# Kernel tuning notes

Hardware: AMD Instinct MI355X
Metric: run time of the kernel (lower is better)

The kernel has to match this reference:

```python
import jax, jax.numpy as jnp
import numpy as np

EPS = 1e-10
BETA = 1.0  # beta passed to VectorQuantizer in Encoder_conv


def _conv(x, w, b, stride, pad):
    # x: NCHW, w: OIHW
    y = jax.lax.conv_general_dilated(x, w, window_strides=stride, padding=pad,
                                     dimension_numbers=('NCHW', 'OIHW', 'NCHW'))
    if b is not None:
        y = y + b[None, :, None, None]
    return y


def _forward(x, w_in, b_in, w_h1, b_h1, w_h2, b_h2, w_h3, b_h3,
             r0_w1, r0_w2, r1_w1, r1_w2, emb):
    relu = jax.nn.relu
    h = relu(_conv(x, w_in, b_in, (2, 2), [(1, 1), (1, 1)]))      # [B,128,256,256]
    h = relu(_conv(h, w_h1, b_h1, (4, 4), [(2, 2), (2, 2)]))      # [B,256,64,64]
    h = relu(_conv(h, w_h2, b_h2, (4, 4), [(2, 2), (2, 2)]))      # [B,256,16,16]
    h = relu(_conv(h, w_h3, b_h3, (2, 2), [(1, 1), (1, 1)]))      # [B,256,8,8]
    # ResidualBlock with 2 Residual layers: relu->conv[1,3]->relu->conv[1,1], no bias
    for wa, wb in ((r0_w1, r0_w2), (r1_w1, r1_w2)):
        t = _conv(relu(h), wa, None, (1, 1), [(0, 0), (1, 1)])
        t = _conv(relu(t), wb, None, (1, 1), [(0, 0), (0, 0)])
        h = h + t
    h = relu(h)
    # VectorQuantizer
    lat = jnp.transpose(h, (0, 2, 3, 1))                          # [B,H,W,D]
    D = emb.shape[1]
    flat = lat.reshape(-1, D)                                     # [N,D]
    dist = (jnp.sum(flat * flat, axis=1, keepdims=True)
            + jnp.sum(emb * emb, axis=1)
            - 2.0 * flat @ emb.T)                                 # [N,K]
    idx = jnp.argmin(dist, axis=1)                                # [N]
    quant = emb[idx].reshape(lat.shape)                           # [B,H,W,D]
    sg = jax.lax.stop_gradient
    e_loss = jnp.mean((sg(quant) - lat) ** 2)
    q_loss = jnp.mean((quant - sg(lat)) ** 2)
    loss = q_loss + BETA * e_loss
    quant_st = lat + sg(quant - lat)                              # straight-through
    probs = jnp.mean(jax.nn.one_hot(idx, emb.shape[0], dtype=lat.dtype), axis=0)
    perplexity = jnp.exp(-jnp.sum(probs * jnp.log(probs + EPS)))
    return jnp.transpose(quant_st, (0, 3, 1, 2)), loss, perplexity


def setup_inputs() -> dict:
    key = jax.random.key(0)
    ks = jax.random.split(key, 14)
    C_in, C, K = 3, 256, 512
    s = 0.05
    f32 = jnp.float32
    return {
        'x':     jax.random.normal(ks[0], (8, C_in, 512, 512), f32),
        'w_in':  jax.random.normal(ks[1], (C // 2, C_in, 4, 4), f32) * s,
        'b_in':  jnp.zeros((C // 2,), f32),
        'w_h1':  jax.random.normal(ks[2], (C, C // 2, 7, 7), f32) * s,
        'b_h1':  jnp.zeros((C,), f32),
        'w_h2':  jax.random.normal(ks[3], (C, C, 7, 7), f32) * s,
        'b_h2':  jnp.zeros((C,), f32),
        'w_h3':  jax.random.normal(ks[4], (C, C, 3, 3), f32) * s,
        'b_h3':  jnp.zeros((C,), f32),
        'r0_w1': jax.random.normal(ks[5], (4 * C, C, 1, 3), f32) * s,
        'r0_w2': jax.random.normal(ks[6], (C, 4 * C, 1, 1), f32) * s,
        'r1_w1': jax.random.normal(ks[7], (4 * C, C, 1, 3), f32) * s,
        'r1_w2': jax.random.normal(ks[8], (C, 4 * C, 1, 1), f32) * s,
        'emb':   jax.random.uniform(ks[9], (K, C), f32, -1.0 / K, 1.0 / K),
    }


def reference(x, w_in, b_in, w_h1, b_h1, w_h2, b_h2, w_h3, b_h3,
              r0_w1, r0_w2, r1_w1, r1_w2, emb):
    return _forward(x, w_in, b_in, w_h1, b_h1, w_h2, b_h2, w_h3, b_h3,
                    r0_w1, r0_w2, r1_w1, r1_w2, emb)
```

## Files before the change

kernel.cpp:

```cpp
#include <hip/hip_runtime.h>
#include <hip/hip_bf16.h>

typedef __hip_bfloat16 bf16;
typedef __attribute__((ext_vector_type(4))) float f32x4;
typedef __attribute__((ext_vector_type(8))) short short8;

__device__ __forceinline__ float b2f(bf16 v) { return __bfloat162float(v); }
__device__ __forceinline__ ushort f2bu(float v)
{
    bf16 b = __float2bfloat16(v);
    return *(ushort*)&b;
}
__device__ __forceinline__ uint relu2(uint v)
{
    uint r = v;
    if (r & 0x8000u)     r &= 0xFFFF0000u;
    if (r & 0x80000000u) r &= 0x0000FFFFu;
    return r;
}
__device__ __forceinline__ uint packbf2(float a, float b)
{
    uint lo = f2bu(a), hi = f2bu(b);
    return lo | (hi << 16);
}

typedef const __attribute__((address_space(1))) unsigned int* as1_u32;
typedef __attribute__((address_space(3))) unsigned int* as3_u32;
__device__ __forceinline__ void gld16(const void* g, uint* l)
{
    __builtin_amdgcn_global_load_lds((as1_u32)g, (as3_u32)l, 16, 0, 0);
}

__global__ __launch_bounds__(256) void initw_k(
        const float* __restrict__ w_in, const float* __restrict__ w_h1,
        const float* __restrict__ w_h2, const float* __restrict__ w_h3,
        const float* __restrict__ r0w1, const float* __restrict__ r0w2,
        const float* __restrict__ r1w1, const float* __restrict__ r1w2,
        const float* __restrict__ emb,
        bf16* __restrict__ wp1, bf16* __restrict__ wpack2, bf16* __restrict__ wpack3,
        bf16* __restrict__ wp4, bf16* __restrict__ wpA0, bf16* __restrict__ wpA1,
        bf16* __restrict__ wpB0, bf16* __restrict__ wpB1,
        float* __restrict__ en, float* __restrict__ mse, int* __restrict__ hist,
        float* __restrict__ zpad)
{
    __shared__ ushort ls[12544];
    int b = blockIdx.x, t = threadIdx.x;

    if (b < 256) {
        const float* src = w_h1 + (size_t)b * 6272;
        for (int i = t; i < 6272; i += 256) ls[i] = f2bu(src[i]);
        __syncthreads();
        for (int e = t; e < 800; e += 256) {
            int tap = e >> 4, cib8 = e & 15;
            short8 v;
            #pragma unroll
            for (int cil = 0; cil < 8; ++cil)
                v[cil] = (tap < 49) ? (short)ls[(cib8 * 8 + cil) * 49 + tap] : (short)0;
            *(short8*)(wpack2 + ((size_t)(tap * 16 + cib8) * 256 + b) * 8) = v;
        }
        return;
    }
    if (b < 512) {
        int co = b - 256;
        const float* src = w_h2 + (size_t)co * 12544;
        for (int i = t; i < 12544; i += 256) ls[i] = f2bu(src[i]);
        __syncthreads();
        for (int e = t; e < 1600; e += 256) {
            int tap = e >> 5, cib8 = e & 31;
            short8 v;
            #pragma unroll
            for (int cil = 0; cil < 8; ++cil)
                v[cil] = (tap < 49) ? (short)ls[(cib8 * 8 + cil) * 49 + tap] : (short)0;
            *(short8*)(wpack3 + ((size_t)(tap * 32 + cib8) * 256 + co) * 8) = v;
        }
        return;
    }
    if (b < 768) {
        int co = b - 512;
        const float* src = w_h3 + (size_t)co * 2304;
        for (int i = t; i < 2304; i += 256) ls[i] = f2bu(src[i]);
        __syncthreads();
        for (int e = t; e < 288; e += 256) {
            int tap = e >> 5, cib8 = e & 31;
            short8 v;
            #pragma unroll
            for (int cil = 0; cil < 8; ++cil)
                v[cil] = (short)ls[(cib8 * 8 + cil) * 9 + tap];
            *(short8*)(wp4 + ((size_t)(tap * 32 + cib8) * 256 + co) * 8) = v;
        }
        return;
    }
    if (b < 2816) {
        int r = b - 768;
        int which = r >> 10;
        int co = r & 1023;
        const float* srcb = which ? r1w1 : r0w1;
        bf16* dstb = which ? wpA1 : wpA0;
        const float* src = srcb + (size_t)co * 768;
        for (int i = t; i < 768; i += 256) ls[i] = f2bu(src[i]);
        __syncthreads();
        if (t < 96) {
            int tap = t >> 5, cib8 = t & 31;
            short8 v;
            #pragma unroll
            for (int cil = 0; cil < 8; ++cil)
                v[cil] = (short)ls[(cib8 * 8 + cil) * 3 + tap];
            *(short8*)(dstb + ((size_t)(tap * 32 + cib8) * 1024 + co) * 8) = v;
        }
        return;
    }
    if (b < 3072) {
        int r = b - 2816;
        int which = r >> 7;
        const float* srcb = which ? r1w2 : r0w2;
        bf16* dstb = which ? wpB1 : wpB0;
        int c = (r & 127) * 256 + t;
        int cib8 = c >> 8, co = c & 255;
        const float* s = srcb + (size_t)co * 1024 + cib8 * 8;
        short8 v;
        #pragma unroll
        for (int cil = 0; cil < 8; ++cil) v[cil] = (short)f2bu(s[cil]);
        *(short8*)(dstb + (size_t)c * 8) = v;
        return;
    }
    if (b < 3104) {
        int i = (b - 3072) * 256 + t;
        int j = i & 7; int co = (i >> 3) & 127; int kb = i >> 10;
        int k = kb * 8 + j;
        wp1[i] = __float2bfloat16(k < 48 ? w_in[co * 48 + k] : 0.f);
        return;
    }
    if (b < 3106) {
        int row = (b - 3104) * 256 + t;
        const float4* e = (const float4*)(emb + (size_t)row * 256);
        float s = 0.f;
        for (int d4 = 0; d4 < 64; ++d4) {
            float4 v = e[d4];
            s += v.x * v.x + v.y * v.y + v.z * v.z + v.w * v.w;
        }
        en[row] = s;
        return;
    }
    if (t == 0) mse[0] = 0.f;
    for (int i = t; i < 512; i += 256) hist[i] = 0;
    if (t < 64) zpad[t] = 0.f;
}

__global__ __launch_bounds__(256) void conv1m_k(const float* __restrict__ x,
        const bf16* __restrict__ wp1, const float* __restrict__ bias,
        bf16* __restrict__ h1c)
{
    int bid = blockIdx.x;
    int pxt = bid & 511, img = bid >> 9;
    int tr = pxt >> 4, tc = pxt & 15;
    int oh0 = tr * 8, ow0 = tc * 16;
    const float* xi = x + (size_t)img * 786432;
    bf16* oT = h1c + (size_t)img * 8388608;

    int t = threadIdx.x;
    int wave = t >> 6, lane = t & 63;
    int quad = lane >> 4, l15 = lane & 15;

    __shared__ ushort xs[4 * 640];
    __shared__ ushort ot[128 * 136];

    int ihb = oh0 * 2 - 1, iwb = ow0 * 2 - 1;
    for (int i = t; i < 1836; i += 256) {
        int ci = i / 612; int r1 = i - ci * 612;
        int ihl = r1 / 34, iwl = r1 - ihl * 34;
        int ih = ihb + ihl, iw = iwb + iwl;
        float v = 0.f;
        if ((unsigned)ih < 512u && (unsigned)iw < 512u)
            v = xi[ci * 262144 + ih * 512 + iw];
        xs[ci * 640 + ihl * 35 + iwl] = f2bu(v);
    }
    for (int i = t; i < 640; i += 256) xs[3 * 640 + i] = 0;
    __syncthreads();

    f32x4 zero = {0.f, 0.f, 0.f, 0.f};
    f32x4 acc[8][2];
    #pragma unroll
    for (int m = 0; m < 8; ++m) { acc[m][0] = zero; acc[m][1] = zero; }

    int ci_b = quad >> 1;
    int kh0 = (quad & 1) * 2;
    int iwl0 = 2 * l15;

    #pragma unroll
    for (int ks = 0; ks < 2; ++ks) {
        union { short8 v; uint u[4]; } b[2];
        #pragma unroll
        for (int nt = 0; nt < 2; ++nt) {
            int py = wave * 2 + nt;
            int base = (ks * 2 + ci_b) * 640 + (2 * py + kh0) * 35 + iwl0;
            b[nt].u[0] = *(const uint*)&xs[base];
            b[nt].u[1] = *(const uint*)&xs[base + 2];
            b[nt].u[2] = *(const uint*)&xs[base + 35];
            b[nt].u[3] = *(const uint*)&xs[base + 37];
        }
        const bf16* abase = wp1 + ((size_t)(ks * 4 + quad) * 128 + l15) * 8;
        #pragma unroll
        for (int m = 0; m < 8; ++m) {
            short8 a = *(const short8*)(abase + m * 16 * 8);
            acc[m][0] = __builtin_amdgcn_mfma_f32_16x16x32_bf16(a, b[0].v, acc[m][0], 0, 0, 0);
            acc[m][1] = __builtin_amdgcn_mfma_f32_16x16x32_bf16(a, b[1].v, acc[m][1], 0, 0, 0);
        }
    }

    #pragma unroll
    for (int m = 0; m < 8; ++m) {
        int cobase = m * 16 + quad * 4;
        float b0 = bias[cobase], b1 = bias[cobase + 1];
        float b2 = bias[cobase + 2], b3 = bias[cobase + 3];
        #pragma unroll
        for (int nt = 0; nt < 2; ++nt) {
            int pxl = (wave * 2 + nt) * 16 + l15;
            uint w0 = packbf2(fmaxf(b0 + acc[m][nt][0], 0.f),
                              fmaxf(b1 + acc[m][nt][1], 0.f));
            uint w1 = packbf2(fmaxf(b2 + acc[m][nt][2], 0.f),
                              fmaxf(b3 + acc[m][nt][3], 0.f));
            *(uint*)&ot[pxl * 136 + cobase]     = w0;
            *(uint*)&ot[pxl * 136 + cobase + 2] = w1;
        }
    }
    __syncthreads();
    {
        int pxl = t >> 1, half = t & 1;
        int oh = oh0 + (pxl >> 4), ow = ow0 + (pxl & 15);
        size_t px = (size_t)(oh * 256 + ow);
        #pragma unroll
        for (int cb = 0; cb < 4; ++cb) {
            int c16 = half * 4 + cb;
            const uint4* src = (const uint4*)&ot[pxl * 136 + c16 * 16];
            uint4* dst = (uint4*)(oT + ((size_t)c16 * 65536 + px) * 16);
            dst[0] = src[0];
            dst[1] = src[1];
        }
    }
}

template <int IH, int OH, int CI, int SPLIT, int MODE>
__global__ __launch_bounds__(256, 2) void conv_mfma9_k(
        const bf16* __restrict__ inC, const bf16* __restrict__ wpack,
        const float* __restrict__ bias, float* __restrict__ outA,
        bf16* __restrict__ outT, const float* __restrict__ zpad)
{
    constexpr int TPD = OH / 8;
    constexpr int NT = TPD * TPD;
    constexpr int CPB = (CI / 16) / SPLIT;
    constexpr int CIB8 = CI / 8;
    constexpr int NPX = IH * IH;
    constexpr int SLOTS = 2496;

    int bid = blockIdx.x;
    int pxt = bid % NT;
    int rest = bid / NT;
    int img = rest & 7;
    int split = rest >> 3;
    int oh0 = (pxt / TPD) * 8, ow0 = (pxt % TPD) * 8;

    int t = threadIdx.x;
    int wave = t >> 6, lane = t & 63;
    int quad = lane >> 4, l15 = lane & 15;

    const bf16* inb = inC + (size_t)img * ((size_t)NPX * CI);

    __shared__ __align__(16) uint bufA[SLOTS * 4];
    __shared__ __align__(16) uint bufB[SLOTS * 4];

    f32x4 zero = {0.f, 0.f, 0.f, 0.f};
    f32x4 acc[4][4];
    #pragma unroll
    for (int a = 0; a < 4; ++a)
        #pragma unroll
        for (int b = 0; b < 4; ++b) acc[a][b] = zero;

    int ihb = oh0 * 4 - 2, iwb = ow0 * 4 - 2;
    int qxl = l15 & 7, pyl = l15 >> 3;
    int tap_par = quad >> 1, ci_half = quad & 1;

    int  srel[10];
    bool sval[10];
    #pragma unroll
    for (int it = 0; it < 10; ++it) {
        int sb = (it < 9) ? it * 256 + wave * 64 : 2304 + wave * 64;
        int p  = sb + lane;
        int pb = p << 4;
        int lb = pb ^ (((pb >> 7) & 7) << 4);
        int j  = lb >> 4;
        int pos = j >> 1, half = j & 1;
        int r = pos / 35, c = pos - r * 35;
        int ih = ihb + r, iw = iwb + c;
        sval[it] = (j < 2450) && ((unsigned)ih < (unsigned)IH)
                   && ((unsigned)iw < (unsigned)IH);
        srel[it] = (ih * IH + iw) * 16 + half * 8;
    }

    auto stage = [&](int ch, uint* dst) {
        const bf16* cbp = inb + (size_t)ch * NPX * 16;
        #pragma unroll
        for (int it = 0; it < 10; ++it) {
            if (it == 9 && wave >= 3) continue;
            int sb = (it < 9) ? it * 256 + wave * 64 : 2304 + wave * 64;
            const void* src = sval[it] ? (const void*)(cbp + srel[it])
                                       : (const void*)zpad;
            gld16(src, dst + sb * 4);
        }
    };

    int rbase = pyl * 4480 + qxl * 128 + ci_half * 16;
    int d1  = tap_par * 32;
    int d29 = tap_par * 928;

    auto compute = [&](int ch, const uint* cbuf) {
        const bf16* ab = wpack
            + ((size_t)(ch * 2 + ci_half) * 256 + wave * 64 + l15) * 8
            + (size_t)tap_par * (CIB8 * 2048);
        __builtin_amdgcn_s_setprio(1);
        short8 aC[4], bC[4], aN[4], bN[4];
        {
            #pragma unroll
            for (int ct = 0; ct < 4; ++ct)
                aC[ct] = *(const short8*)(ab + ct * 128);
            int lbb = rbase + d1;
            #pragma unroll
            for (int pt = 0; pt < 4; ++pt) {
                int lb = lbb + pt * 8960;
                int pb = lb ^ (((lb >> 7) & 7) << 4);
                bC[pt] = *(const short8*)((const char*)cbuf + pb);
            }
        }
        #pragma unroll
        for (int tp = 0; tp < 25; ++tp) {
            if (tp < 24) {
                const int tn  = tp + 1;
                const int kh0 = (2 * tn) / 7, kw0 = (2 * tn) % 7;
                const int cE  = (kh0 * 35 + kw0) * 32;
                int dsel = (tn == 24) ? 0 : ((kw0 == 6) ? d29 : d1);
                int lbb  = rbase + cE + dsel;
                const bf16* at = ab + (size_t)(2 * tn) * (CIB8 * 2048);
                #pragma unroll
                for (int ct = 0; ct < 4; ++ct)
                    aN[ct] = *(const short8*)(at + ct * 128);
                #pragma unroll
                for (int pt = 0; pt < 4; ++pt) {
                    int lb = lbb + pt * 8960;
                    int pb = lb ^ (((lb >> 7) & 7) << 4);
                    bN[pt] = *(const short8*)((const char*)cbuf + pb);
                }
            }
            #pragma unroll
            for (int pt = 0; pt < 4; ++pt)
                #pragma unroll
                for (int ct = 0; ct < 4; ++ct)
                    acc[ct][pt] = __builtin_amdgcn_mfma_f32_16x16x32_bf16(
                        aC[ct], bC[pt], acc[ct][pt], 0, 0, 0);
            if (tp < 24) {
                #pragma unroll
                for (int i = 0; i < 4; ++i) { aC[i] = aN[i]; bC[i] = bN[i]; }
            }
        }
        __builtin_amdgcn_s_setprio(0);
    };

    if constexpr (CPB == 1) {
        stage(split, bufA);
        __syncthreads();
        compute(split, bufA);
    } else {
        stage(split * CPB, bufA);
        __syncthreads();
        for (int cc2 = 0; cc2 < CPB; cc2 += 2) {
            stage(split * CPB + cc2 + 1, bufB);
            compute(split * CPB + cc2, bufA);
            __syncthreads();
            if (cc2 + 2 < CPB) stage(split * CPB + cc2 + 2, bufA);
            compute(split * CPB + cc2 + 1, bufB);
            __syncthreads();
        }
    }

    #pragma unroll
    for (int ct = 0; ct < 4; ++ct) {
        int cobase = wave * 64 + ct * 16 + quad * 4;
        #pragma unroll
        for (int pt = 0; pt < 4; ++pt) {
            int px = pt * 16 + l15;
            int oh = oh0 + (px >> 3), ow = ow0 + (px & 7);
            int pxg = oh * OH + ow;
            #pragma unroll
            for (int r = 0; r < 4; ++r) {
                int co = cobase + r;
                float v = acc[ct][pt][r];
                if (MODE == 3) {
                    outA[(size_t)split * ((size_t)8 * OH * OH * 256)
                         + (size_t)img * (OH * OH * 256)
                         + (size_t)co * (OH * OH) + pxg] = v;
                } else {
                    float o = fmaxf(bias[co] + v, 0.f);
                    size_t base = (size_t)img * (size_t)(OH * OH * 256);
                    outT[base + ((size_t)(co >> 4) * (OH * OH) + pxg) * 16 + (co & 15)]
                        = __float2bfloat16(o);
                }
            }
        }
    }
}

__global__ void combine3_k(const float* __restrict__ p3, const float* __restrict__ bias,
                           bf16* __restrict__ h3T)
{
    int idx = blockIdx.x * 256 + threadIdx.x;
    int px = idx & 255;
    int co = (idx >> 8) & 255;
    int img = idx >> 16;
    float v = bias[co];
    #pragma unroll
    for (int s = 0; s < 16; ++s) v += p3[(size_t)s * 524288 + idx];
    v = fmaxf(v, 0.f);
    h3T[((size_t)img * 256 + px) * 256 + co] = __float2bfloat16(v);
}

__global__ __launch_bounds__(256) void conv4m_k(const bf16* __restrict__ h3T,
        const bf16* __restrict__ wp4, const float* __restrict__ bias,
        bf16* __restrict__ h4T)
{
    int bid = blockIdx.x;
    int img = bid >> 2, cog = bid & 3;
    int t = threadIdx.x;
    int wave = t >> 6, lane = t & 63;
    int quad = lane >> 4, l15 = lane & 15;

    __shared__ uint pt[16 * 325];

    for (int i = t; i < 16 * 325; i += 256) pt[i] = 0;

    f32x4 zero = {0.f, 0.f, 0.f, 0.f};
    f32x4 acc[4];
    #pragma unroll
    for (int b = 0; b < 4; ++b) acc[b] = zero;

    const bf16* inb = h3T + (size_t)img * 65536;

    for (int ch = 0; ch < 8; ++ch) {
        __syncthreads();
        for (int e = t; e < 4096; e += 256) {
            int cp = e & 15, px = e >> 4;
            int py = px >> 4, qx = px & 15;
            uint v = *(const uint*)(inb + (size_t)px * 256 + ch * 32 + cp * 2);
            pt[cp * 325 + (py + 1) * 18 + qx + 1] = v;
        }
        __syncthreads();

        for (int tap = 0; tap < 9; ++tap) {
            int kh = tap / 3, kw = tap - kh * 3;
            const bf16* abase = wp4 + ((size_t)((tap * 32 + ch * 4 + quad) * 256)
                                       + cog * 64 + wave * 16 + l15) * 8;
            short8 a = *(const short8*)abase;
            #pragma unroll
            for (int pq = 0; pq < 4; ++pq) {
                int pyo = 2 * pq + (l15 >> 3);
                int ipos = (2 * pyo + kh) * 18 + 2 * (l15 & 7) + kw;
                union { short8 v; uint u[4]; } b;
                b.u[0] = pt[(quad * 4 + 0) * 325 + ipos];
                b.u[1] = pt[(quad * 4 + 1) * 325 + ipos];
                b.u[2] = pt[(quad * 4 + 2) * 325 + ipos];
                b.u[3] = pt[(quad * 4 + 3) * 325 + ipos];
                acc[pq] = __builtin_amdgcn_mfma_f32_16x16x32_bf16(
                    a, b.v, acc[pq], 0, 0, 0);
            }
        }
    }

    int cobase = cog * 64 + wave * 16 + quad * 4;
    #pragma unroll
    for (int pq = 0; pq < 4; ++pq) {
        int px = pq * 16 + l15;
        #pragma unroll
        for (int r = 0; r < 4; ++r) {
            int co = cobase + r;
            float v = fmaxf(bias[co] + acc[pq][r], 0.f);
            h4T[((size_t)img * 64 + px) * 256 + co] = __float2bfloat16(v);
        }
    }
}

__global__ __launch_bounds__(256) void resam_k(const bf16* __restrict__ hT,
        const bf16* __restrict__ wpA, bf16* __restrict__ t1T)
{
    int bid = blockIdx.x;
    int img = bid >> 3, g = bid & 7;
    int t = threadIdx.x;
    int wave = t >> 6, lane = t & 63;
    int quad = lane >> 4, l15 = lane & 15;

    __shared__ uint ph[128 * 81];

    for (int i = t; i < 128 * 81; i += 256) ph[i] = 0;
    __syncthreads();
    const bf16* inb = hT + (size_t)img * 16384;
    for (int e = t; e < 8192; e += 256) {
        int cp = e & 127, px = e >> 7;
        uint v = relu2(*(const uint*)(inb + (size_t)px * 256 + cp * 2));
        ph[cp * 81 + (px >> 3) * 10 + (px & 7) + 1] = v;
    }
    __syncthreads();

    f32x4 zero = {0.f, 0.f, 0.f, 0.f};
    f32x4 acc[2][4];
    #pragma unroll
    for (int a = 0; a < 2; ++a)
        #pragma unroll
        for (int b = 0; b < 4; ++b) acc[a][b] = zero;

    for (int ch = 0; ch < 8; ++ch) {
        for (int tap = 0; tap < 3; ++tap) {
            const bf16* abase = wpA + ((size_t)(tap * 32 + ch * 4 + quad) * 1024
                                       + g * 128 + wave * 32 + l15) * 8;
            short8 a[2];
            #pragma unroll
            for (int ct = 0; ct < 2; ++ct)
                a[ct] = *(const short8*)(abase + ct * 16 * 8);
            #pragma unroll
            for (int pq = 0; pq < 4; ++pq) {
                int py = 2 * pq + (l15 >> 3);
                int pos = py * 10 + (l15 & 7) + tap;
                union { short8 v; uint u[4]; } b;
                b.u[0] = ph[(ch * 16 + quad * 4 + 0) * 81 + pos];
                b.u[1] = ph[(ch * 16 + quad * 4 + 1) * 81 + pos];
                b.u[2] = ph[(ch * 16 + quad * 4 + 2) * 81 + pos];
                b.u[3] = ph[(ch * 16 + quad * 4 + 3) * 81 + pos];
                #pragma unroll
                for (int ct = 0; ct < 2; ++ct)
                    acc[ct][pq] = __builtin_amdgcn_mfma_f32_16x16x32_bf16(
                        a[ct], b.v, acc[ct][pq], 0, 0, 0);
            }
        }
    }

    #pragma unroll
    for (int ct = 0; ct < 2; ++ct) {
        int cobase = g * 128 + wave * 32 + ct * 16 + quad * 4;
        #pragma unroll
        for (int pq = 0; pq < 4; ++pq) {
            int px = pq * 16 + l15;
            #pragma unroll
            for (int r = 0; r < 4; ++r)
                t1T[((size_t)img * 64 + px) * 1024 + cobase + r]
                    = __float2bfloat16(acc[ct][pq][r]);
        }
    }
}

__global__ __launch_bounds__(256) void resbm_k(const bf16* __restrict__ holdT,
        const bf16* __restrict__ t1T, const bf16* __restrict__ wpB,
        bf16* __restrict__ hnewT)
{
    int bid = blockIdx.x;
    int img = bid >> 2, cog = bid & 3;
    int t = threadIdx.x;
    int wave = t >> 6, lane = t & 63;
    int quad = lane >> 4, l15 = lane & 15;

    __shared__ uint pb[256 * 65];

    f32x4 zero = {0.f, 0.f, 0.f, 0.f};
    f32x4 acc[4];
    #pragma unroll
    for (int b = 0; b < 4; ++b) acc[b] = zero;

    const bf16* inb = t1T + (size_t)img * 65536;

    for (int s = 0; s < 2; ++s) {
        __syncthreads();
        for (int e = t; e < 16384; e += 256) {
            int cp = e & 255, px = e >> 8;
            uint v = relu2(*(const uint*)(inb + (size_t)px * 1024 + s * 512 + cp * 2));
            pb[cp * 65 + px] = v;
        }
        __syncthreads();

        for (int chl = 0; chl < 16; ++chl) {
            int ch = s * 16 + chl;
            const bf16* abase = wpB + ((size_t)(ch * 4 + quad) * 256
                                       + cog * 64 + wave * 16 + l15) * 8;
            short8 a = *(const short8*)abase;
            #pragma unroll
            for (int pq = 0; pq < 4; ++pq) {
                int px = pq * 16 + l15;
                union { short8 v; uint u[4]; } b;
                b.u[0] = pb[(chl * 16 + quad * 4 + 0) * 65 + px];
                b.u[1] = pb[(chl * 16 + quad * 4 + 1) * 65 + px];
                b.u[2] = pb[(chl * 16 + quad * 4 + 2) * 65 + px];
                b.u[3] = pb[(chl * 16 + quad * 4 + 3) * 65 + px];
                acc[pq] = __builtin_amdgcn_mfma_f32_16x16x32_bf16(
                    a, b.v, acc[pq], 0, 0, 0);
            }
        }
    }

    int cobase = cog * 64 + wave * 16 + quad * 4;
    #pragma unroll
    for (int pq = 0; pq < 4; ++pq) {
        int px = pq * 16 + l15;
        #pragma unroll
        for (int r = 0; r < 4; ++r) {
            int co = cobase + r;
            size_t o = ((size_t)img * 64 + px) * 256 + co;
            float v = b2f(holdT[o]) + acc[pq][r];
            hnewT[o] = __float2bfloat16(v);
        }
    }
}

__global__ __launch_bounds__(256) void vq_k(const bf16* __restrict__ h6T,
        const float* __restrict__ emb, const float* __restrict__ en,
        float* __restrict__ out, float* __restrict__ mse_acc, int* __restrict__ hist)
{
    int row0 = blockIdx.x * 4;
    int t = threadIdx.x;
    int wave = t >> 6, lane = t & 63;
    __shared__ float lat[4][256];
    __shared__ float swd[4][4];
    __shared__ int   swi[4][4];
    __shared__ int   fidx[4];
    __shared__ float smse[4];

    for (int e = t; e < 1024; e += 256) {
        int r = e >> 8, c = e & 255;
        lat[r][c] = fmaxf(b2f(h6T[(size_t)(row0 + r) * 256 + c]), 0.f);
    }
    __syncthreads();

    float a0[4] = {0.f, 0.f, 0.f, 0.f}, a1[4] = {0.f, 0.f, 0.f, 0.f};
    const float4* e0 = (const float4*)(emb + (size_t)t * 256);
    const float4* e1 = (const float4*)(emb + (size_t)(t + 256) * 256);
    for (int d4 = 0; d4 < 64; ++d4) {
        float4 v0 = e0[d4], v1 = e1[d4];
        #pragma unroll
        for (int r = 0; r < 4; ++r) {
            float l0 = lat[r][d4 * 4], l1 = lat[r][d4 * 4 + 1];
            float l2 = lat[r][d4 * 4 + 2], l3 = lat[r][d4 * 4 + 3];
            a0[r] += l0 * v0.x + l1 * v0.y + l2 * v0.z + l3 * v0.w;
            a1[r] += l0 * v1.x + l1 * v1.y + l2 * v1.z + l3 * v1.w;
        }
    }
    float en0 = en[t], en1 = en[t + 256];
    float bd[4]; int bi[4];
    #pragma unroll
    for (int r = 0; r < 4; ++r) {
        float d0 = en0 - 2.f * a0[r], d1v = en1 - 2.f * a1[r];
        bd[r] = d0; bi[r] = t;
        if (d1v < bd[r]) { bd[r] = d1v; bi[r] = t + 256; }
    }
    #pragma unroll
    for (int s = 1; s < 64; s <<= 1) {
        #pragma unroll
        for (int r = 0; r < 4; ++r) {
            float od = __shfl_xor(bd[r], s);
            int   oi = __shfl_xor(bi[r], s);
            if (od < bd[r] || (od == bd[r] && oi < bi[r])) { bd[r] = od; bi[r] = oi; }
        }
    }
    if (lane == 0) {
        #pragma unroll
        for (int r = 0; r < 4; ++r) { swd[wave][r] = bd[r]; swi[wave][r] = bi[r]; }
    }
    __syncthreads();
    if (t < 4) {
        float best = swd[0][t]; int bidx = swi[0][t];
        for (int w = 1; w < 4; ++w) {
            float od = swd[w][t]; int oi = swi[w][t];
            if (od < best || (od == best && oi < bidx)) { best = od; bidx = oi; }
        }
        fidx[t] = bidx;
    }
    __syncthreads();

    float msel = 0.f;
    #pragma unroll
    for (int r = 0; r < 4; ++r) {
        int row = row0 + r;
        int b = row >> 6, y = (row >> 3) & 7, xx = row & 7;
        float q = emb[(size_t)fidx[r] * 256 + t];
        out[((size_t)(b * 256 + t) * 8 + y) * 8 + xx] = q;
        float diff = q - lat[r][t];
        msel += diff * diff;
    }
    #pragma unroll
    for (int s = 1; s < 64; s <<= 1) msel += __shfl_xor(msel, s);
    if (lane == 0) smse[wave] = msel;
    __syncthreads();
    if (t == 0) atomicAdd(mse_acc, smse[0] + smse[1] + smse[2] + smse[3]);
    if (t < 4) atomicAdd(&hist[fidx[t]], 1);
}

__global__ void final_k(const float* __restrict__ mse_acc, const int* __restrict__ hist,
                        float* __restrict__ out)
{
    __shared__ float sh[512];
    int t = threadIdx.x;
    float p = (float)hist[t] / 512.f;
    sh[t] = p * logf(p + 1e-10f);
    __syncthreads();
    for (int s = 256; s > 0; s >>= 1) {
        if (t < s) sh[t] += sh[t + s];
        __syncthreads();
    }
    if (t == 0) {
        float loss = 2.f * mse_acc[0] / (512.f * 256.f);
        float perp = expf(-sh[0]);
        out[131072] = loss;
        out[131073] = perp;
    }
}

extern "C" void kernel_launch(void* const* d_in, const int* in_sizes, int n_in,
                              void* d_out, int out_size, void* d_ws, size_t ws_size,
                              hipStream_t stream)
{
    const float* x    = (const float*)d_in[0];
    const float* w_in = (const float*)d_in[1];
    const float* b_in = (const float*)d_in[2];
    const float* w_h1 = (const float*)d_in[3];
    const float* b_h1 = (const float*)d_in[4];
    const float* w_h2 = (const float*)d_in[5];
    const float* b_h2 = (const float*)d_in[6];
    const float* w_h3 = (const float*)d_in[7];
    const float* b_h3 = (const float*)d_in[8];
    const float* r0w1 = (const float*)d_in[9];
    const float* r0w2 = (const float*)d_in[10];
    const float* r1w1 = (const float*)d_in[11];
    const float* r1w2 = (const float*)d_in[12];
    const float* emb  = (const float*)d_in[13];
    float* out = (float*)d_out;

    char* ws = (char*)d_ws;
    size_t off = 0;
    auto alloc = [&](size_t bytes) -> void* {
        void* p = ws + off;
        off += (bytes + 255) & ~(size_t)255;
        return p;
    };

    float* en  = (float*)alloc(512 * 4);
    float* mse = (float*)alloc(256);
    int*  hist = (int*)alloc(512 * 4);
    float* zpad = (float*)alloc(256);
    float* p3  = (float*)alloc(8388608ull * 4);
    bf16* h3T  = (bf16*)alloc(524288ull * 2);
    bf16* h4T  = (bf16*)alloc(131072ull * 2);
    bf16* t1T  = (bf16*)alloc(524288ull * 2);
    bf16* h5T  = (bf16*)alloc(131072ull * 2);
    bf16* h6T  = (bf16*)alloc(131072ull * 2);
    bf16* wp1  = (bf16*)alloc(8192ull * 2);
    bf16* wpack2 = (bf16*)alloc(1638400ull * 2);
    bf16* wpack3 = (bf16*)alloc(3276800ull * 2);
    bf16* wp4  = (bf16*)alloc(589824ull * 2);
    bf16* wpA0 = (bf16*)alloc(786432ull * 2);
    bf16* wpA1 = (bf16*)alloc(786432ull * 2);
    bf16* wpB0 = (bf16*)alloc(262144ull * 2);
    bf16* wpB1 = (bf16*)alloc(262144ull * 2);
    bf16* h2c  = (bf16*)alloc(8388608ull * 2);
    size_t base_end = off;

    const size_t H1F_B = 8388608ull * 8 * 2;
    size_t needT1 = base_end + H1F_B + 4096;
    bf16* h1c;
    int tier;
    if (ws_size >= needT1) {
        h1c = (bf16*)alloc(H1F_B);
        tier = 1;
    } else {
        h1c = (bf16*)alloc(8388608ull * 2);
        tier = 2;
    }

    initw_k<<<3107, 256, 0, stream>>>(w_in, w_h1, w_h2, w_h3, r0w1, r0w2, r1w1, r1w2,
        emb, wp1, wpack2, wpack3, wp4, wpA0, wpA1, wpB0, wpB1, en, mse, hist, zpad);

    if (tier == 1) {
        conv1m_k<<<4096, 256, 0, stream>>>(x, wp1, b_in, h1c);
        conv_mfma9_k<256, 64, 128, 1, 0><<<512, 256, 0, stream>>>(
            h1c, wpack2, b_h1, nullptr, h2c, zpad);
    } else {
        for (int n = 0; n < 8; ++n) {
            conv1m_k<<<512, 256, 0, stream>>>(x + (size_t)n * 786432, wp1, b_in, h1c);
            conv_mfma9_k<256, 64, 128, 1, 0><<<64, 256, 0, stream>>>(
                h1c, wpack2, b_h1, nullptr, h2c + (size_t)n * 1048576, zpad);
        }
    }

    conv_mfma9_k<64, 16, 256, 16, 3><<<512, 256, 0, stream>>>(
        h2c, wpack3, nullptr, p3, nullptr, zpad);
    combine3_k<<<2048, 256, 0, stream>>>(p3, b_h2, h3T);

    conv4m_k<<<32, 256, 0, stream>>>(h3T, wp4, b_h3, h4T);
    resam_k<<<64, 256, 0, stream>>>(h4T, wpA0, t1T);
    resbm_k<<<32, 256, 0, stream>>>(h4T, t1T, wpB0, h5T);
    resam_k<<<64, 256, 0, stream>>>(h5T, wpA1, t1T);
    resbm_k<<<32, 256, 0, stream>>>(h5T, t1T, wpB1, h6T);

    vq_k<<<128, 256, 0, stream>>>(h6T, emb, en, out, mse, hist);
    final_k<<<1, 512, 0, stream>>>(mse, hist, out);
}
```

Baseline: 464.4 us.

## Fuse tail stages into one persistent kernel with grid barriers, halve conv3 split-K

Replaces the chain of small tail kernels (combine, conv4, two residual blocks, VQ, final reduction) with a single 64-block persistent kernel that uses a global atomic barrier between stages. The goal is to remove repeated launch overhead and inter-kernel gaps on small, latency-bound stages. It also reduces conv3's split-K from 16 to 8 and halves the partial-sum buffer, giving fewer but longer conv3 blocks. The combine step now transposes through LDS. The spin barrier relies on all 64 blocks being co-resident, and the VQ stage now runs on 64 blocks instead of 128.

```diff
diff --git a/kernel.cpp b/kernel.cpp
--- a/kernel.cpp
+++ b/kernel.cpp
@@ -29,6 +29,28 @@
 __device__ __forceinline__ void gld16(const void* g, uint* l)
 {
     __builtin_amdgcn_global_load_lds((as1_u32)g, (as3_u32)l, 16, 0, 0);
+}
+
+__device__ __forceinline__ void gbar(int* bar, int nblk)
+{
+    __syncthreads();
+    if (threadIdx.x == 0) {
+        __threadfence();
+        int g = __hip_atomic_load(&bar[1], __ATOMIC_RELAXED, __HIP_MEMORY_SCOPE_AGENT);
+        int a = __hip_atomic_fetch_add(&bar[0], 1, __ATOMIC_ACQ_REL, __HIP_MEMORY_SCOPE_AGENT);
+        if (a == nblk - 1) {
+            __hip_atomic_store(&bar[0], 0, __ATOMIC_RELAXED, __HIP_MEMORY_SCOPE_AGENT);
+            __hip_atomic_store(&bar[1], g + 1, __ATOMIC_RELEASE, __HIP_MEMORY_SCOPE_AGENT);
+        } else {
+            for (int it = 0; it < (1 << 22); ++it) {
+                if (__hip_atomic_load(&bar[1], __ATOMIC_ACQUIRE,
+                                      __HIP_MEMORY_SCOPE_AGENT) != g) break;
+                __builtin_amdgcn_s_sleep(8);
+            }
+        }
+        __threadfence();
+    }
+    __syncthreads();
 }
 
 __global__ __launch_bounds__(256) void initw_k(
@@ -41,7 +63,7 @@
         bf16* __restrict__ wp4, bf16* __restrict__ wpA0, bf16* __restrict__ wpA1,
         bf16* __restrict__ wpB0, bf16* __restrict__ wpB1,
         float* __restrict__ en, float* __restrict__ mse, int* __restrict__ hist,
-        float* __restrict__ zpad)
+        float* __restrict__ zpad, int* __restrict__ bar)
 {
     __shared__ ushort ls[12544];
     int b = blockIdx.x, t = threadIdx.x;
@@ -144,6 +166,7 @@
     if (t == 0) mse[0] = 0.f;
     for (int i = t; i < 512; i += 256) hist[i] = 0;
     if (t < 64) zpad[t] = 0.f;
+    if (t < 2) bar[t] = 0;
 }
 
 __global__ __launch_bounds__(256) void conv1m_k(const float* __restrict__ x,
@@ -407,311 +430,307 @@
     }
 }
 
-__global__ void combine3_k(const float* __restrict__ p3, const float* __restrict__ bias,
-                           bf16* __restrict__ h3T)
-{
-    int idx = blockIdx.x * 256 + threadIdx.x;
-    int px = idx & 255;
-    int co = (idx >> 8) & 255;
-    int img = idx >> 16;
-    float v = bias[co];
-    #pragma unroll
-    for (int s = 0; s < 16; ++s) v += p3[(size_t)s * 524288 + idx];
-    v = fmaxf(v, 0.f);
-    h3T[((size_t)img * 256 + px) * 256 + co] = __float2bfloat16(v);
-}
-
-__global__ __launch_bounds__(256) void conv4m_k(const bf16* __restrict__ h3T,
-        const bf16* __restrict__ wp4, const float* __restrict__ bias,
-        bf16* __restrict__ h4T)
-{
-    int bid = blockIdx.x;
-    int img = bid >> 2, cog = bid & 3;
-    int t = threadIdx.x;
+__global__ __launch_bounds__(256) void tail_k(
+        const float* __restrict__ p3, const float* __restrict__ bias2,
+        bf16* __restrict__ h3T,
+        const bf16* __restrict__ wp4, const float* __restrict__ bias3,
+        bf16* __restrict__ h4T,
+        const bf16* __restrict__ wpA0, const bf16* __restrict__ wpA1,
+        bf16* __restrict__ t1T,
+        const bf16* __restrict__ wpB0, const bf16* __restrict__ wpB1,
+        bf16* __restrict__ h5T, bf16* __restrict__ h6T,
+        const float* __restrict__ emb, const float* __restrict__ en,
+        float* __restrict__ out, float* __restrict__ mse_acc,
+        int* __restrict__ hist, int* __restrict__ bar)
+{
+    __shared__ uint smem[16640];
+    int bid = blockIdx.x, t = threadIdx.x;
     int wave = t >> 6, lane = t & 63;
     int quad = lane >> 4, l15 = lane & 15;
-
-    __shared__ uint pt[16 * 325];
-
-    for (int i = t; i < 16 * 325; i += 256) pt[i] = 0;
-
     f32x4 zero = {0.f, 0.f, 0.f, 0.f};
-    f32x4 acc[4];
-    #pragma unroll
-    for (int b = 0; b < 4; ++b) acc[b] = zero;
-
-    const bf16* inb = h3T + (size_t)img * 65536;
-
-    for (int ch = 0; ch < 8; ++ch) {
+
+    {
+        int img = bid >> 3, px0 = (bid & 7) * 32;
+        ushort* lds = (ushort*)smem;
+        int pxl = t & 31, coq = t >> 5;
+        for (int cb = 0; cb < 32; ++cb) {
+            int co = cb * 8 + coq;
+            const float* src = p3 + ((size_t)img * 256 + co) * 256 + px0 + pxl;
+            float v = bias2[co];
+            #pragma unroll
+            for (int s = 0; s < 8; ++s) v += src[(size_t)s * 524288];
+            lds[pxl * 264 + co] = f2bu(fmaxf(v, 0.f));
+        }
         __syncthreads();
-        for (int e = t; e < 4096; e += 256) {
-            int cp = e & 15, px = e >> 4;
-            int py = px >> 4, qx = px & 15;
-            uint v = *(const uint*)(inb + (size_t)px * 256 + ch * 32 + cp * 2);
-            pt[cp * 325 + (py + 1) * 18 + qx + 1] = v;
-        }
-        __syncthreads();
-
-        for (int tap = 0; tap < 9; ++tap) {
-            int kh = tap / 3, kw = tap - kh * 3;
-            const bf16* abase = wp4 + ((size_t)((tap * 32 + ch * 4 + quad) * 256)
-                                       + cog * 64 + wave * 16 + l15) * 8;
-            short8 a = *(const short8*)abase;
-            #pragma unroll
-            for (int pq = 0; pq < 4; ++pq) {
-                int pyo = 2 * pq + (l15 >> 3);
-                int ipos = (2 * pyo + kh) * 18 + 2 * (l15 & 7) + kw;
-                union { short8 v; uint u[4]; } b;
-                b.u[0] = pt[(quad * 4 + 0) * 325 + ipos];
-                b.u[1] = pt[(quad * 4 + 1) * 325 + ipos];
-                b.u[2] = pt[(quad * 4 + 2) * 325 + ipos];
-                b.u[3] = pt[(quad * 4 + 3) * 325 + ipos];
-                acc[pq] = __builtin_amdgcn_mfma_f32_16x16x32_bf16(
-                    a, b.v, acc[pq], 0, 0, 0);
-            }
-        }
-    }
-
-    int cobase = cog * 64 + wave * 16 + quad * 4;
-    #pragma unroll
-    for (int pq = 0; pq < 4; ++pq) {
-        int px = pq * 16 + l15;
-        #pragma unroll
-        for (int r = 0; r < 4; ++r) {
-            int co = cobase + r;
-            float v = fmaxf(bias[co] + acc[pq][r], 0.f);
-            h4T[((size_t)img * 64 + px) * 256 + co] = __float2bfloat16(v);
-        }
-    }
-}
-
-__global__ __launch_bounds__(256) void resam_k(const bf16* __restrict__ hT,
-        const bf16* __restrict__ wpA, bf16* __restrict__ t1T)
-{
-    int bid = blockIdx.x;
-    int img = bid >> 3, g = bid & 7;
-    int t = threadIdx.x;
-    int wave = t >> 6, lane = t & 63;
-    int quad = lane >> 4, l15 = lane & 15;
-
-    __shared__ uint ph[128 * 81];
-
-    for (int i = t; i < 128 * 81; i += 256) ph[i] = 0;
-    __syncthreads();
-    const bf16* inb = hT + (size_t)img * 16384;
-    for (int e = t; e < 8192; e += 256) {
-        int cp = e & 127, px = e >> 7;
-        uint v = relu2(*(const uint*)(inb + (size_t)px * 256 + cp * 2));
-        ph[cp * 81 + (px >> 3) * 10 + (px & 7) + 1] = v;
-    }
-    __syncthreads();
-
-    f32x4 zero = {0.f, 0.f, 0.f, 0.f};
-    f32x4 acc[2][4];
-    #pragma unroll
-    for (int a = 0; a < 2; ++a)
-        #pragma unroll
-        for (int b = 0; b < 4; ++b) acc[a][b] = zero;
-
-    for (int ch = 0; ch < 8; ++ch) {
-        for (int tap = 0; tap < 3; ++tap) {
-            const bf16* abase = wpA + ((size_t)(tap * 32 + ch * 4 + quad) * 1024
-                                       + g * 128 + wave * 32 + l15) * 8;
-            short8 a[2];
-            #pragma unroll
-            for (int ct = 0; ct < 2; ++ct)
-                a[ct] = *(const short8*)(abase + ct * 16 * 8);
-            #pragma unroll
-            for (int pq = 0; pq < 4; ++pq) {
-                int py = 2 * pq + (l15 >> 3);
-                int pos = py * 10 + (l15 & 7) + tap;
-                union { short8 v; uint u[4]; } b;
-                b.u[0] = ph[(ch * 16 + quad * 4 + 0) * 81 + pos];
-                b.u[1] = ph[(ch * 16 + quad * 4 + 1) * 81 + pos];
-                b.u[2] = ph[(ch * 16 + quad * 4 + 2) * 81 + pos];
-                b.u[3] = ph[(ch * 16 + quad * 4 + 3) * 81 + pos];
-                #pragma unroll
-                for (int ct = 0; ct < 2; ++ct)
-                    acc[ct][pq] = __builtin_amdgcn_mfma_f32_16x16x32_bf16(
-                        a[ct], b.v, acc[ct][pq], 0, 0, 0);
-            }
-        }
-    }
-
-    #pragma unroll
-    for (int ct = 0; ct < 2; ++ct) {
-        int cobase = g * 128 + wave * 32 + ct * 16 + quad * 4;
+        int co8 = (t & 31) * 8;
+        #pragma unroll
+        for (int pp = 0; pp < 4; ++pp) {
+            int p2 = pp * 8 + (t >> 5);
+            short8 v = *(const short8*)&lds[p2 * 264 + co8];
+            *(short8*)(h3T + ((size_t)img * 256 + px0 + p2) * 256 + co8) = v;
+        }
+    }
+    gbar(bar, 64);
+
+    if (bid < 32) {
+        int img = bid >> 2, cog = bid & 3;
+        uint* pt = smem;
+        for (int i = t; i < 16 * 325; i += 256) pt[i] = 0;
+        f32x4 acc[4];
+        #pragma unroll
+        for (int b = 0; b < 4; ++b) acc[b] = zero;
+        const bf16* inb = h3T + (size_t)img * 65536;
+        for (int ch = 0; ch < 8; ++ch) {
+            __syncthreads();
+            for (int e = t; e < 4096; e += 256) {
+                int cp = e & 15, px = e >> 4;
+                int py = px >> 4, qx = px & 15;
+                uint v = *(const uint*)(inb + (size_t)px * 256 + ch * 32 + cp * 2);
+                pt[cp * 325 + (py + 1) * 18 + qx + 1] = v;
+            }
+            __syncthreads();
+            for (int tap = 0; tap < 9; ++tap) {
+                int kh = tap / 3, kw = tap - kh * 3;
+                const bf16* abase = wp4 + ((size_t)((tap * 32 + ch * 4 + quad) * 256)
+                                           + cog * 64 + wave * 16 + l15) * 8;
+                short8 a = *(const short8*)abase;
+                #pragma unroll
+                for (int pq = 0; pq < 4; ++pq) {
+                    int pyo = 2 * pq + (l15 >> 3);
+                    int ipos = (2 * pyo + kh) * 18 + 2 * (l15 & 7) + kw;
+                    union { short8 v; uint u[4]; } b;
+                    b.u[0] = pt[(quad * 4 + 0) * 325 + ipos];
+                    b.u[1] = pt[(quad * 4 + 1) * 325 + ipos];
+                    b.u[2] = pt[(quad * 4 + 2) * 325 + ipos];
+                    b.u[3] = pt[(quad * 4 + 3) * 325 + ipos];
+                    acc[pq] = __builtin_amdgcn_mfma_f32_16x16x32_bf16(
+                        a, b.v, acc[pq], 0, 0, 0);
+                }
+            }
+        }
+        int cobase = cog * 64 + wave * 16 + quad * 4;
         #pragma unroll
         for (int pq = 0; pq < 4; ++pq) {
             int px = pq * 16 + l15;
             #pragma unroll
-            for (int r = 0; r < 4; ++r)
-                t1T[((size_t)img * 64 + px) * 1024 + cobase + r]
-                    = __float2bfloat16(acc[ct][pq][r]);
-        }
-    }
-}
-
-__global__ __launch_bounds__(256) void resbm_k(const bf16* __restrict__ holdT,
-        const bf16* __restrict__ t1T, const bf16* __restrict__ wpB,
-        bf16* __restrict__ hnewT)
-{
-    int bid = blockIdx.x;
-    int img = bid >> 2, cog = bid & 3;
-    int t = threadIdx.x;
-    int wave = t >> 6, lane = t & 63;
-    int quad = lane >> 4, l15 = lane & 15;
-
-    __shared__ uint pb[256 * 65];
-
-    f32x4 zero = {0.f, 0.f, 0.f, 0.f};
-    f32x4 acc[4];
-    #pragma unroll
-    for (int b = 0; b < 4; ++b) acc[b] = zero;
-
-    const bf16* inb = t1T + (size_t)img * 65536;
-
-    for (int s = 0; s < 2; ++s) {
-        __syncthreads();
-        for (int e = t; e < 16384; e += 256) {
-            int cp = e & 255, px = e >> 8;
-            uint v = relu2(*(const uint*)(inb + (size_t)px * 1024 + s * 512 + cp * 2));
-            pb[cp * 65 + px] = v;
-        }
-        __syncthreads();
-
-        for (int chl = 0; chl < 16; ++chl) {
-            int ch = s * 16 + chl;
-            const bf16* abase = wpB + ((size_t)(ch * 4 + quad) * 256
-                                       + cog * 64 + wave * 16 + l15) * 8;
-            short8 a = *(const short8*)abase;
+            for (int r = 0; r < 4; ++r) {
+                int co = cobase + r;
+                float v = fmaxf(bias3[co] + acc[pq][r], 0.f);
+                h4T[((size_t)img * 64 + px) * 256 + co] = __float2bfloat16(v);
+            }
+        }
+    }
+    gbar(bar, 64);
+
+    #pragma unroll 1
+    for (int rb = 0; rb < 2; ++rb) {
+        const bf16* hin  = rb ? h5T : h4T;
+        const bf16* wpA  = rb ? wpA1 : wpA0;
+        const bf16* wpB  = rb ? wpB1 : wpB0;
+        bf16* hout = rb ? h6T : h5T;
+
+        {
+            int img = bid >> 3, g = bid & 7;
+            uint* ph = smem;
+            for (int i = t; i < 128 * 81; i += 256) ph[i] = 0;
+            __syncthreads();
+            const bf16* inb = hin + (size_t)img * 16384;
+            for (int e = t; e < 8192; e += 256) {
+                int cp = e & 127, px = e >> 7;
+                uint v = relu2(*(const uint*)(inb + (size_t)px * 256 + cp * 2));
+                ph[cp * 81 + (px >> 3) * 10 + (px & 7) + 1] = v;
+            }
+            __syncthreads();
+            f32x4 acc[2][4];
+            #pragma unroll
+            for (int a = 0; a < 2; ++a)
+                #pragma unroll
+                for (int b = 0; b < 4; ++b) acc[a][b] = zero;
+            for (int ch = 0; ch < 8; ++ch) {
+                for (int tap = 0; tap < 3; ++tap) {
+                    const bf16* abase = wpA + ((size_t)(tap * 32 + ch * 4 + quad) * 1024
+                                               + g * 128 + wave * 32 + l15) * 8;
+                    short8 a[2];
+                    #pragma unroll
+                    for (int ct = 0; ct < 2; ++ct)
+                        a[ct] = *(const short8*)(abase + ct * 16 * 8);
+                    #pragma unroll
+                    for (int pq = 0; pq < 4; ++pq) {
+                        int py = 2 * pq + (l15 >> 3);
+                        int pos = py * 10 + (l15 & 7) + tap;
+                        union { short8 v; uint u[4]; } b;
+                        b.u[0] = ph[(ch * 16 + quad * 4 + 0) * 81 + pos];
+                        b.u[1] = ph[(ch * 16 + quad * 4 + 1) * 81 + pos];
+                        b.u[2] = ph[(ch * 16 + quad * 4 + 2) * 81 + pos];
+                        b.u[3] = ph[(ch * 16 + quad * 4 + 3) * 81 + pos];
+                        #pragma unroll
+                        for (int ct = 0; ct < 2; ++ct)
+                            acc[ct][pq] = __builtin_amdgcn_mfma_f32_16x16x32_bf16(
+                                a[ct], b.v, acc[ct][pq], 0, 0, 0);
+                    }
+                }
+            }
+            #pragma unroll
+            for (int ct = 0; ct < 2; ++ct) {
+                int cobase = g * 128 + wave * 32 + ct * 16 + quad * 4;
+                #pragma unroll
+                for (int pq = 0; pq < 4; ++pq) {
+                    int px = pq * 16 + l15;
+                    #pragma unroll
+                    for (int r = 0; r < 4; ++r)
+                        t1T[((size_t)img * 64 + px) * 1024 + cobase + r]
+                            = __float2bfloat16(acc[ct][pq][r]);
+                }
+            }
+        }
+        gbar(bar, 64);
+
+        if (bid < 32) {
+            int img = bid >> 2, cog = bid & 3;
+            uint* pb = smem;
+            f32x4 acc[4];
+            #pragma unroll
+            for (int b = 0; b < 4; ++b) acc[b] = zero;
+            const bf16* inb = t1T + (size_t)img * 65536;
+            for (int s = 0; s < 2; ++s) {
+                __syncthreads();
+                for (int e = t; e < 16384; e += 256) {
+                    int cp = e & 255, px = e >> 8;
+                    uint v = relu2(*(const uint*)(inb + (size_t)px * 1024 + s * 512 + cp * 2));
+                    pb[cp * 65 + px] = v;
+                }
+                __syncthreads();
+                for (int chl = 0; chl < 16; ++chl) {
+                    int ch = s * 16 + chl;
+                    const bf16* abase = wpB + ((size_t)(ch * 4 + quad) * 256
+                                               + cog * 64 + wave * 16 + l15) * 8;
+                    short8 a = *(const short8*)abase;
+                    #pragma unroll
+                    for (int pq = 0; pq < 4; ++pq) {
+                        int px = pq * 16 + l15;
+                        union { short8 v; uint u[4]; } b;
+                        b.u[0] = pb[(chl * 16 + quad * 4 + 0) * 65 + px];
+                        b.u[1] = pb[(chl * 16 + quad * 4 + 1) * 65 + px];
+                        b.u[2] = pb[(chl * 16 + quad * 4 + 2) * 65 + px];
+                        b.u[3] = pb[(chl * 16 + quad * 4 + 3) * 65 + px];
+                        acc[pq] = __builtin_amdgcn_mfma_f32_16x16x32_bf16(
+                            a, b.v, acc[pq], 0, 0, 0);
+                    }
+                }
+            }
+            int cobase = cog * 64 + wave * 16 + quad * 4;
             #pragma unroll
             for (int pq = 0; pq < 4; ++pq) {
                 int px = pq * 16 + l15;
-                union { short8 v; uint u[4]; } b;
-                b.u[0] = pb[(chl * 16 + quad * 4 + 0) * 65 + px];
-                b.u[1] = pb[(chl * 16 + quad * 4 + 1) * 65 + px];
-                b.u[2] = pb[(chl * 16 + quad * 4 + 2) * 65 + px];
-                b.u[3] = pb[(chl * 16 + quad * 4 + 3) * 65 + px];
-                acc[pq] = __builtin_amdgcn_mfma_f32_16x16x32_bf16(
-                    a, b.v, acc[pq], 0, 0, 0);
-            }
-        }
-    }
-
-    int cobase = cog * 64 + wave * 16 + quad * 4;
-    #pragma unroll
-    for (int pq = 0; pq < 4; ++pq) {
-        int px = pq * 16 + l15;
-        #pragma unroll
-        for (int r = 0; r < 4; ++r) {
-            int co = cobase + r;
-            size_t o = ((size_t)img * 64 + px) * 256 + co;
-            float v = b2f(holdT[o]) + acc[pq][r];
-            hnewT[o] = __float2bfloat16(v);
-        }
-    }
-}
-
-__global__ __launch_bounds__(256) void vq_k(const bf16* __restrict__ h6T,
-        const float* __restrict__ emb, const float* __restrict__ en,
-        float* __restrict__ out, float* __restrict__ mse_acc, int* __restrict__ hist)
-{
-    int row0 = blockIdx.x * 4;
-    int t = threadIdx.x;
-    int wave = t >> 6, lane = t & 63;
-    __shared__ float lat[4][256];
-    __shared__ float swd[4][4];
-    __shared__ int   swi[4][4];
-    __shared__ int   fidx[4];
-    __shared__ float smse[4];
-
-    for (int e = t; e < 1024; e += 256) {
-        int r = e >> 8, c = e & 255;
-        lat[r][c] = fmaxf(b2f(h6T[(size_t)(row0 + r) * 256 + c]), 0.f);
-    }
-    __syncthreads();
-
-    float a0[4] = {0.f, 0.f, 0.f, 0.f}, a1[4] = {0.f, 0.f, 0.f, 0.f};
-    const float4* e0 = (const float4*)(emb + (size_t)t * 256);
-    const float4* e1 = (const float4*)(emb + (size_t)(t + 256) * 256);
-    for (int d4 = 0; d4 < 64; ++d4) {
-        float4 v0 = e0[d4], v1 = e1[d4];
-        #pragma unroll
-        for (int r = 0; r < 4; ++r) {
-            float l0 = lat[r][d4 * 4], l1 = lat[r][d4 * 4 + 1];
-            float l2 = lat[r][d4 * 4 + 2], l3 = lat[r][d4 * 4 + 3];
-            a0[r] += l0 * v0.x + l1 * v0.y + l2 * v0.z + l3 * v0.w;
-            a1[r] += l0 * v1.x + l1 * v1.y + l2 * v1.z + l3 * v1.w;
-        }
-    }
-    float en0 = en[t], en1 = en[t + 256];
-    float bd[4]; int bi[4];
-    #pragma unroll
-    for (int r = 0; r < 4; ++r) {
-        float d0 = en0 - 2.f * a0[r], d1v = en1 - 2.f * a1[r];
-        bd[r] = d0; bi[r] = t;
-        if (d1v < bd[r]) { bd[r] = d1v; bi[r] = t + 256; }
-    }
-    #pragma unroll
-    for (int s = 1; s < 64; s <<= 1) {
-        #pragma unroll
-        for (int r = 0; r < 4; ++r) {
-            float od = __shfl_xor(bd[r], s);
-            int   oi = __shfl_xor(bi[r], s);
-            if (od < bd[r] || (od == bd[r] && oi < bi[r])) { bd[r] = od; bi[r] = oi; }
-        }
-    }
-    if (lane == 0) {
-        #pragma unroll
-        for (int r = 0; r < 4; ++r) { swd[wave][r] = bd[r]; swi[wave][r] = bi[r]; }
-    }
-    __syncthreads();
-    if (t < 4) {
-        float best = swd[0][t]; int bidx = swi[0][t];
-        for (int w = 1; w < 4; ++w) {
-            float od = swd[w][t]; int oi = swi[w][t];
-            if (od < best || (od == best && oi < bidx)) { best = od; bidx = oi; }
-        }
-        fidx[t] = bidx;
-    }
-    __syncthreads();
-
-    float msel = 0.f;
-    #pragma unroll
-    for (int r = 0; r < 4; ++r) {
-        int row = row0 + r;
-        int b = row >> 6, y = (row >> 3) & 7, xx = row & 7;
-        float q = emb[(size_t)fidx[r] * 256 + t];
-        out[((size_t)(b * 256 + t) * 8 + y) * 8 + xx] = q;
-        float diff = q - lat[r][t];
-        msel += diff * diff;
-    }
-    #pragma unroll
-    for (int s = 1; s < 64; s <<= 1) msel += __shfl_xor(msel, s);
-    if (lane == 0) smse[wave] = msel;
-    __syncthreads();
-    if (t == 0) atomicAdd(mse_acc, smse[0] + smse[1] + smse[2] + smse[3]);
-    if (t < 4) atomicAdd(&hist[fidx[t]], 1);
-}
-
-__global__ void final_k(const float* __restrict__ mse_acc, const int* __restrict__ hist,
-                        float* __restrict__ out)
-{
-    __shared__ float sh[512];
-    int t = threadIdx.x;
-    float p = (float)hist[t] / 512.f;
-    sh[t] = p * logf(p + 1e-10f);
-    __syncthreads();
-    for (int s = 256; s > 0; s >>= 1) {
-        if (t < s) sh[t] += sh[t + s];
+                #pragma unroll
+                for (int r = 0; r < 4; ++r) {
+                    int co = cobase + r;
+                    size_t o = ((size_t)img * 64 + px) * 256 + co;
+                    float v = b2f(hin[o]) + acc[pq][r];
+                    hout[o] = __float2bfloat16(v);
+                }
+            }
+        }
+        gbar(bar, 64);
+    }
+
+    {
+        float* lat  = (float*)smem;
+        float* swd  = lat + 1024;
+        int*   swi  = (int*)(swd + 16);
+        int*   fidx = swi + 16;
+        float* smse = (float*)(fidx + 4);
+        for (int pass = 0; pass < 2; ++pass) {
+            int row0 = bid * 8 + pass * 4;
+            __syncthreads();
+            for (int e = t; e < 1024; e += 256) {
+                int r = e >> 8, c = e & 255;
+                lat[r * 256 + c] = fmaxf(b2f(h6T[(size_t)(row0 + r) * 256 + c]), 0.f);
+            }
+            __syncthreads();
+            float a0[4] = {0.f, 0.f, 0.f, 0.f}, a1[4] = {0.f, 0.f, 0.f, 0.f};
+            const float4* e0 = (const float4*)(emb + (size_t)t * 256);
+            const float4* e1 = (const float4*)(emb + (size_t)(t + 256) * 256);
+            for (int d4 = 0; d4 < 64; ++d4) {
+                float4 v0 = e0[d4], v1 = e1[d4];
+                #pragma unroll
+                for (int r = 0; r < 4; ++r) {
+                    float l0 = lat[r * 256 + d4 * 4],     l1 = lat[r * 256 + d4 * 4 + 1];
+                    float l2 = lat[r * 256 + d4 * 4 + 2], l3 = lat[r * 256 + d4 * 4 + 3];
+                    a0[r] += l0 * v0.x + l1 * v0.y + l2 * v0.z + l3 * v0.w;
+                    a1[r] += l0 * v1.x + l1 * v1.y + l2 * v1.z + l3 * v1.w;
+                }
+            }
+            float en0 = en[t], en1 = en[t + 256];
+            float bd[4]; int bi[4];
+            #pragma unroll
+            for (int r = 0; r < 4; ++r) {
+                float d0 = en0 - 2.f * a0[r], d1v = en1 - 2.f * a1[r];
+                bd[r] = d0; bi[r] = t;
+                if (d1v < bd[r]) { bd[r] = d1v; bi[r] = t + 256; }
+            }
+            #pragma unroll
+            for (int s = 1; s < 64; s <<= 1) {
+                #pragma unroll
+                for (int r = 0; r < 4; ++r) {
+                    float od = __shfl_xor(bd[r], s);
+                    int   oi = __shfl_xor(bi[r], s);
+                    if (od < bd[r] || (od == bd[r] && oi < bi[r])) { bd[r] = od; bi[r] = oi; }
+                }
+            }
+            if (lane == 0) {
+                #pragma unroll
+                for (int r = 0; r < 4; ++r) { swd[wave * 4 + r] = bd[r]; swi[wave * 4 + r] = bi[r]; }
+            }
+            __syncthreads();
+            if (t < 4) {
+                float best = swd[t]; int bidx = swi[t];
+                for (int w = 1; w < 4; ++w) {
+                    float od = swd[w * 4 + t]; int oi = swi[w * 4 + t];
+                    if (od < best || (od == best && oi < bidx)) { best = od; bidx = oi; }
+                }
+                fidx[t] = bidx;
+            }
+            __syncthreads();
+            float msel = 0.f;
+            #pragma unroll
+            for (int r = 0; r < 4; ++r) {
+                int row = row0 + r;
+                int b = row >> 6, y = (row >> 3) & 7, xx = row & 7;
+                float q = emb[(size_t)fidx[r] * 256 + t];
+                out[((size_t)(b * 256 + t) * 8 + y) * 8 + xx] = q;
+                float diff = q - lat[r * 256 + t];
+                msel += diff * diff;
+            }
+            #pragma unroll
+            for (int s = 1; s < 64; s <<= 1) msel += __shfl_xor(msel, s);
+            if (lane == 0) smse[wave] = msel;
+            __syncthreads();
+            if (t == 0) atomicAdd(mse_acc, smse[0] + smse[1] + smse[2] + smse[3]);
+            if (t < 4) atomicAdd(&hist[fidx[t]], 1);
+        }
+    }
+    gbar(bar, 64);
+
+    if (bid == 0) {
+        float* sh = (float*)smem;
+        int h0i = __hip_atomic_load(&hist[t],       __ATOMIC_RELAXED, __HIP_MEMORY_SCOPE_AGENT);
+        int h1i = __hip_atomic_load(&hist[t + 256], __ATOMIC_RELAXED, __HIP_MEMORY_SCOPE_AGENT);
+        float p0 = (float)h0i / 512.f;
+        float p1 = (float)h1i / 512.f;
         __syncthreads();
-    }
-    if (t == 0) {
-        float loss = 2.f * mse_acc[0] / (512.f * 256.f);
-        float perp = expf(-sh[0]);
-        out[131072] = loss;
-        out[131073] = perp;
+        sh[t]       = p0 * logf(p0 + 1e-10f);
+        sh[t + 256] = p1 * logf(p1 + 1e-10f);
+        __syncthreads();
+        for (int s = 256; s > 0; s >>= 1) {
+            if (t < s) sh[t] += sh[t + s];
+            __syncthreads();
+        }
+        if (t == 0) {
+            float m = __hip_atomic_load(mse_acc, __ATOMIC_RELAXED, __HIP_MEMORY_SCOPE_AGENT);
+            out[131072] = 2.f * m / (512.f * 256.f);
+            out[131073] = expf(-sh[0]);
+        }
     }
 }
 
@@ -747,7 +766,8 @@
     float* mse = (float*)alloc(256);
     int*  hist = (int*)alloc(512 * 4);
     float* zpad = (float*)alloc(256);
-    float* p3  = (float*)alloc(8388608ull * 4);
+    int*   bar = (int*)alloc(256);
+    float* p3  = (float*)alloc(4194304ull * 4);
     bf16* h3T  = (bf16*)alloc(524288ull * 2);
     bf16* h4T  = (bf16*)alloc(131072ull * 2);
     bf16* t1T  = (bf16*)alloc(524288ull * 2);
@@ -777,7 +797,7 @@
     }
 
     initw_k<<<3107, 256, 0, stream>>>(w_in, w_h1, w_h2, w_h3, r0w1, r0w2, r1w1, r1w2,
-        emb, wp1, wpack2, wpack3, wp4, wpA0, wpA1, wpB0, wpB1, en, mse, hist, zpad);
+        emb, wp1, wpack2, wpack3, wp4, wpA0, wpA1, wpB0, wpB1, en, mse, hist, zpad, bar);
 
     if (tier == 1) {
         conv1m_k<<<4096, 256, 0, stream>>>(x, wp1, b_in, h1c);
@@ -791,16 +811,9 @@
         }
     }
 
-    conv_mfma9_k<64, 16, 256, 16, 3><<<512, 256, 0, stream>>>(
+    conv_mfma9_k<64, 16, 256, 8, 3><<<256, 256, 0, stream>>>(
         h2c, wpack3, nullptr, p3, nullptr, zpad);
-    combine3_k<<<2048, 256, 0, stream>>>(p3, b_h2, h3T);
-
-    conv4m_k<<<32, 256, 0, stream>>>(h3T, wp4, b_h3, h4T);
-    resam_k<<<64, 256, 0, stream>>>(h4T, wpA0, t1T);
-    resbm_k<<<32, 256, 0, stream>>>(h4T, t1T, wpB0, h5T);
-    resam_k<<<64, 256, 0, stream>>>(h5T, wpA1, t1T);
-    resbm_k<<<32, 256, 0, stream>>>(h5T, t1T, wpB1, h6T);
-
-    vq_k<<<128, 256, 0, stream>>>(h6T, emb, en, out, mse, hist);
-    final_k<<<1, 512, 0, stream>>>(mse, hist, out);
-}
+
+    tail_k<<<64, 256, 0, stream>>>(p3, b_h2, h3T, wp4, b_h3, h4T,
+        wpA0, wpA1, t1T, wpB0, wpB1, h5T, h6T, emb, en, out, mse, hist, bar);
+}
```

After: 511.0 us. 10.0% more time.
